# Performance work log

Hardware: AMD Instinct MI355X
Metric: run time of the kernel (lower is better)

Reference implementation:

```python
import jax, jax.numpy as jnp
import numpy as np

B, D, V = 2048, 512, 50304


def setup_inputs() -> dict:
    key = jax.random.key(0)
    ks = jax.random.split(key, 7)
    scale = 1.0 / np.sqrt(D)
    return {
        "student_h": jax.random.normal(ks[0], (B, D), dtype=jnp.float32) * scale,
        "student_c": jax.random.normal(ks[1], (V, D), dtype=jnp.float32) * scale,
        "teacher_h": jax.random.normal(ks[2], (B, D), dtype=jnp.float32) * scale,
        "teacher_c": jax.random.normal(ks[3], (V, D), dtype=jnp.float32) * scale,
        "ce_coeff": jax.random.uniform(ks[4], (B,), dtype=jnp.float32),
        "kl_coeff": jax.random.uniform(ks[5], (B,), dtype=jnp.float32),
        "targets": jax.random.randint(ks[6], (B,), 0, V, dtype=jnp.int64),
    }


def reference(student_h, student_c, teacher_h, teacher_c, ce_coeff, kl_coeff, targets):
    # Fused linear head: student/teacher logits over the full vocab  [B, V]
    s_logits = jnp.einsum("bd,vd->bv", student_h, student_c)
    t_logits = jnp.einsum("bd,vd->bv", teacher_h, teacher_c)

    s_lse = jax.nn.logsumexp(s_logits, axis=1)  # [B]
    t_lse = jax.nn.logsumexp(t_logits, axis=1)  # [B]

    # Cross-entropy per row: lse - logit[target]
    tgt_logit = jnp.take_along_axis(s_logits, targets[:, None], axis=1)[:, 0]
    ce = s_lse - tgt_logit  # [B]

    # KL(teacher || student) per row
    log_ps = s_logits - s_lse[:, None]
    log_pt = t_logits - t_lse[:, None]
    pt = jnp.exp(log_pt)
    kl = jnp.sum(pt * (log_pt - log_ps), axis=1)  # [B]

    # Per-row coefficients absorb any reduction weighting (as in the kernel)
    loss = jnp.sum(ce_coeff * ce + kl_coeff * kl)
    return loss
```

## Files before the change

kernel.cpp:

```cpp
#include <hip/hip_runtime.h>
#include <hip/hip_fp8.h>

#define B_ 2048
#define D_ 512
#define V_ 50304
#define NROWB 16
#define NCOLB 393
#define NWG (NROWB * NCOLB)
#define NCOPY 32
#define LOG2E 1.44269504088896340736f
#define LN2 0.69314718055994530942f

typedef __attribute__((ext_vector_type(16))) float f32x16;
typedef __attribute__((ext_vector_type(8))) int v8i;
typedef unsigned char u8;

__device__ inline unsigned f2bf(float f) {
  unsigned u = __float_as_uint(f);
  u += 0x7fffu + ((u >> 16) & 1u);
  return u >> 16;
}

__global__ void cast8t_kernel(const float* __restrict__ src, uint4* __restrict__ dst,
                              float scale, int nchunk) {
  int i = blockIdx.x * blockDim.x + threadIdx.x;
  if (i >= nchunk) return;
  int c = i & 127;
  int h = (i >> 7) & 1;
  int kc = (i >> 8) & 7;
  int p = i >> 11;
  const float4* s = (const float4*)(src + (size_t)(p * 128 + c) * 512 + kc * 64 + h * 32);
  union { u8 b[32]; uint4 u[2]; } o;
#pragma unroll
  for (int q = 0; q < 8; ++q) {
    float4 f = s[q];
    o.b[q * 4 + 0] = __hip_fp8_e4m3(f.x * scale).__x;
    o.b[q * 4 + 1] = __hip_fp8_e4m3(f.y * scale).__x;
    o.b[q * 4 + 2] = __hip_fp8_e4m3(f.z * scale).__x;
    o.b[q * 4 + 3] = __hip_fp8_e4m3(f.w * scale).__x;
  }
  dst[2 * i] = o.u[0];
  dst[2 * i + 1] = o.u[1];
}

__global__ void cast8_kernel(const float* __restrict__ src, uint2* __restrict__ dst,
                             float scale, int n8) {
  int i = blockIdx.x * blockDim.x + threadIdx.x;
  int stride = gridDim.x * blockDim.x;
  const float4* s4 = (const float4*)src;
  for (; i < n8; i += stride) {
    float4 a = s4[2 * i], b = s4[2 * i + 1];
    union { u8 c[8]; uint2 u; } p;
    p.c[0] = __hip_fp8_e4m3(a.x * scale).__x;
    p.c[1] = __hip_fp8_e4m3(a.y * scale).__x;
    p.c[2] = __hip_fp8_e4m3(a.z * scale).__x;
    p.c[3] = __hip_fp8_e4m3(a.w * scale).__x;
    p.c[4] = __hip_fp8_e4m3(b.x * scale).__x;
    p.c[5] = __hip_fp8_e4m3(b.y * scale).__x;
    p.c[6] = __hip_fp8_e4m3(b.z * scale).__x;
    p.c[7] = __hip_fp8_e4m3(b.w * scale).__x;
    dst[i] = p.u;
  }
}

__global__ void tgt_kernel(const float* __restrict__ sh, const float* __restrict__ sc,
                           const int* __restrict__ targets, float* __restrict__ tgt_out) {
  int gid = blockIdx.x * blockDim.x + threadIdx.x;
  int w = gid >> 6, lane = gid & 63;
  if (w >= B_) return;
  int tgt = targets[w];
  const float4* a = (const float4*)(sh + (size_t)w * D_);
  const float4* b = (const float4*)(sc + (size_t)tgt * D_);
  float acc = 0.f;
#pragma unroll
  for (int i = 0; i < 2; ++i) {
    float4 x = a[lane + i * 64], y = b[lane + i * 64];
    acc += x.x * y.x + x.y * y.y + x.z * y.z + x.w * y.w;
  }
#pragma unroll
  for (int off = 1; off < 64; off <<= 1) acc += __shfl_xor(acc, off);
  if (lane == 0) tgt_out[w] = acc;
}

__global__ __launch_bounds__(512, 4) void lce_main(
    const u8* __restrict__ SH8, const u8* __restrict__ TH8,
    const u8* __restrict__ SC8t, const u8* __restrict__ TC8t,
    float* __restrict__ stats32) {
  __shared__ __align__(16) uint exch[8192];
  __shared__ float pss[2][2][64];
  __shared__ float pst[2][2][64];
  __shared__ float pat[2][2][64];

  const int tid = threadIdx.x;
  const int lane = tid & 63, w = tid >> 6;
  const int wq = w & 3;
  const int mat = w >> 2;
  const int wr = wq >> 1;
  const int wc = wq & 1;
  const int l5 = lane & 31;
  const int hi = lane >> 5;

  const int hw = blockIdx.x;
  const int lid = (hw & 7) * 786 + (hw >> 3);
  const int row0 = (lid & 15) * 128;
  const int p = lid >> 4;
  const int jcopy = (hw & 7) * 4 + (p & 3);
  float* stats = stats32 + (size_t)jcopy * B_ * 3;

  const u8* gA = (mat ? TH8 : SH8) + (size_t)(row0 + wr * 64 + l5) * D_ + hi * 32;
  const u8* gB = (mat ? TC8t : SC8t) + (size_t)p * 65536 + hi * 4096 + (wc * 64 + l5) * 32;

  f32x16 acc[2][2];
#pragma unroll
  for (int mi = 0; mi < 2; ++mi)
#pragma unroll
    for (int ni = 0; ni < 2; ++ni)
#pragma unroll
      for (int e = 0; e < 16; ++e) acc[mi][ni][e] = 0.f;

#pragma unroll
  for (int kc = 0; kc < 8; ++kc) {
    v8i av[2], bv[2];
#pragma unroll
    for (int mi = 0; mi < 2; ++mi)
      av[mi] = *(const v8i*)(gA + (size_t)(mi * 32) * D_ + kc * 64);
#pragma unroll
    for (int ni = 0; ni < 2; ++ni)
      bv[ni] = *(const v8i*)(gB + kc * 8192 + ni * 1024);

    __builtin_amdgcn_s_setprio(1);
#pragma unroll
    for (int mi = 0; mi < 2; ++mi)
#pragma unroll
      for (int ni = 0; ni < 2; ++ni)
        acc[mi][ni] = __builtin_amdgcn_mfma_scale_f32_32x32x64_f8f6f4(
            av[mi], bv[ni], acc[mi][ni], 0, 0, 0, 127, 0, 127);
    __builtin_amdgcn_s_setprio(0);
  }

  const float inv = 1.0f / 256.0f;

  if (mat == 0) {
#pragma unroll
    for (int mi = 0; mi < 2; ++mi)
#pragma unroll
      for (int ni = 0; ni < 2; ++ni)
#pragma unroll
        for (int rp = 0; rp < 8; ++rp) {
          uint u = f2bf(acc[mi][ni][2 * rp] * inv) |
                   (f2bf(acc[mi][ni][2 * rp + 1] * inv) << 16);
          exch[(((wq * 2 + mi) * 2 + ni) * 8 + rp) * 64 + lane] = u;
        }
  }
  __syncthreads();

  if (mat == 0) {
#pragma unroll
    for (int mi = 0; mi < 2; ++mi)
#pragma unroll
      for (int rp = 0; rp < 8; ++rp) {
        float v0 = __builtin_amdgcn_exp2f(acc[mi][0][2 * rp] * inv) +
                   __builtin_amdgcn_exp2f(acc[mi][1][2 * rp] * inv);
        float v1 = __builtin_amdgcn_exp2f(acc[mi][0][2 * rp + 1] * inv) +
                   __builtin_amdgcn_exp2f(acc[mi][1][2 * rp + 1] * inv);
#pragma unroll
        for (int off = 1; off < 32; off <<= 1) {
          v0 += __shfl_xor(v0, off);
          v1 += __shfl_xor(v1, off);
        }
        if (l5 == 0) {
          int r0 = ((2 * rp) & 3) + 8 * (rp >> 1) + 4 * hi + mi * 32;
          pss[wr][wc][r0] = v0;
          pss[wr][wc][r0 + 1] = v1;
        }
      }
  } else {
#pragma unroll
    for (int mi = 0; mi < 2; ++mi)
#pragma unroll
      for (int rp = 0; rp < 8; ++rp) {
        float st0 = 0.f, st1 = 0.f, at0 = 0.f, at1 = 0.f;
#pragma unroll
        for (int ni = 0; ni < 2; ++ni) {
          uint u = exch[(((wq * 2 + mi) * 2 + ni) * 8 + rp) * 64 + lane];
          float sv0 = __uint_as_float(u << 16);
          float sv1 = __uint_as_float(u & 0xffff0000u);
          float t0 = acc[mi][ni][2 * rp] * inv;
          float t1 = acc[mi][ni][2 * rp + 1] * inv;
          float e0 = __builtin_amdgcn_exp2f(t0);
          float e1 = __builtin_amdgcn_exp2f(t1);
          st0 += e0; st1 += e1;
          at0 += e0 * (t0 - sv0);
          at1 += e1 * (t1 - sv1);
        }
#pragma unroll
        for (int off = 1; off < 32; off <<= 1) {
          st0 += __shfl_xor(st0, off);
          st1 += __shfl_xor(st1, off);
          at0 += __shfl_xor(at0, off);
          at1 += __shfl_xor(at1, off);
        }
        if (l5 == 0) {
          int r0 = ((2 * rp) & 3) + 8 * (rp >> 1) + 4 * hi + mi * 32;
          pst[wr][wc][r0] = st0;
          pst[wr][wc][r0 + 1] = st1;
          pat[wr][wc][r0] = at0;
          pat[wr][wc][r0 + 1] = at1;
        }
      }
  }
  __syncthreads();

  if (wc == 0) {
    int row = row0 + wr * 64 + lane;
    if (mat == 0) {
      float ss = pss[wr][0][lane] + pss[wr][1][lane];
      atomicAdd(&stats[(size_t)row * 3 + 0], ss);
    } else {
      float st = pst[wr][0][lane] + pst[wr][1][lane];
      float at = pat[wr][0][lane] + pat[wr][1][lane];
      atomicAdd(&stats[(size_t)row * 3 + 1], st);
      atomicAdd(&stats[(size_t)row * 3 + 2], at);
    }
  }
}

__global__ void finalize(const float* __restrict__ stats32, const float* __restrict__ tgt,
                         const float* __restrict__ cec, const float* __restrict__ klc,
                         float* __restrict__ out) {
  __shared__ float red[16];
  int tid = threadIdx.x;
  float acc = 0.f;
  for (int r = tid; r < B_; r += 1024) {
    float ss = 0.f, st = 0.f, at = 0.f;
#pragma unroll
    for (int j = 0; j < NCOPY; ++j) {
      const float* s = stats32 + ((size_t)j * B_ + r) * 3;
      ss += s[0]; st += s[1]; at += s[2];
    }
    float s_lse = LN2 * __builtin_amdgcn_logf(ss);
    float t_lse = LN2 * __builtin_amdgcn_logf(st);
    float kl = s_lse - t_lse + LN2 * at / st;
    float ce = s_lse - tgt[r];
    acc += cec[r] * ce + klc[r] * kl;
  }
#pragma unroll
  for (int off = 1; off < 64; off <<= 1) acc += __shfl_xor(acc, off);
  if ((tid & 63) == 0) red[tid >> 6] = acc;
  __syncthreads();
  if (tid == 0) {
    float s = 0.f;
#pragma unroll
    for (int i = 0; i < 16; ++i) s += red[i];
    out[0] = s;
  }
}

extern "C" void kernel_launch(void* const* d_in, const int* in_sizes, int n_in,
                              void* d_out, int out_size, void* d_ws, size_t ws_size,
                              hipStream_t stream) {
  const float* sh = (const float*)d_in[0];
  const float* sc = (const float*)d_in[1];
  const float* th = (const float*)d_in[2];
  const float* tc = (const float*)d_in[3];
  const float* cec = (const float*)d_in[4];
  const float* klc = (const float*)d_in[5];
  const int* targets = (const int*)d_in[6];
  float* out = (float*)d_out;

  char* ws = (char*)d_ws;
  u8* SC8t = (u8*)ws;
  u8* TC8t = SC8t + (size_t)V_ * D_;
  u8* SH8 = TC8t + (size_t)V_ * D_;
  u8* TH8 = SH8 + (size_t)B_ * D_;
  float* stats32 = (float*)(TH8 + (size_t)B_ * D_);
  float* tgt = stats32 + (size_t)NCOPY * B_ * 3;

  hipMemsetAsync(stats32, 0, (size_t)NCOPY * B_ * 3 * sizeof(float), stream);
  const float hscale = 16.0f * LOG2E;
  const float cscale = 16.0f;
  const int nchunk = V_ * D_ / 32;
  cast8t_kernel<<<3144, 256, 0, stream>>>(sc, (uint4*)SC8t, cscale, nchunk);
  cast8t_kernel<<<3144, 256, 0, stream>>>(tc, (uint4*)TC8t, cscale, nchunk);
  cast8_kernel<<<256, 256, 0, stream>>>(sh, (uint2*)SH8, hscale, B_ * D_ / 8);
  cast8_kernel<<<256, 256, 0, stream>>>(th, (uint2*)TH8, hscale, B_ * D_ / 8);
  tgt_kernel<<<512, 256, 0, stream>>>(sh, sc, targets, tgt);

  lce_main<<<NWG, 512, 0, stream>>>(SH8, TH8, SC8t, TC8t, stats32);
  finalize<<<1, 1024, 0, stream>>>(stats32, tgt, cec, klc, out);
}
```

Before: 318.6 us.

## Fuse student/teacher GEMMs per wave with LDS double-buffered vocab tiles

The main kernel moves from 512-thread blocks, where separate waves computed the student and teacher tiles and swapped bf16 logits through LDS, to 256-thread blocks in which each wave computes both the student and teacher accumulators for the same tile. The epilogue then needs no cross-wave exchange. Each block now covers three vocab panels in sequence. Vocab tiles are staged into double-buffered LDS with global_load_lds, using manual vmcnt waits and barriers, and the hidden-state matrices use the same transposed fp8 layout so the cast kernel can be reused. This removes the bf16 rounding of student logits and the LDS exchange, and amortises block launch. In exchange it roughly doubles accumulator register pressure, issues more atomics per wave, and depends on hand-written waitcnt counts being correct.

Measured after the change: 1.103 ms. 3.46x slower.

```diff
diff --git a/kernel.cpp b/kernel.cpp
--- a/kernel.cpp
+++ b/kernel.cpp
@@ -4,9 +4,8 @@
 #define B_ 2048
 #define D_ 512
 #define V_ 50304
-#define NROWB 16
-#define NCOLB 393
-#define NWG (NROWB * NCOLB)
+#define NPG 131
+#define NWG (16 * NPG)
 #define NCOPY 32
 #define LOG2E 1.44269504088896340736f
 #define LN2 0.69314718055994530942f
@@ -15,10 +14,9 @@
 typedef __attribute__((ext_vector_type(8))) int v8i;
 typedef unsigned char u8;
 
-__device__ inline unsigned f2bf(float f) {
-  unsigned u = __float_as_uint(f);
-  u += 0x7fffu + ((u >> 16) & 1u);
-  return u >> 16;
+__device__ inline void gload16(const void* g, void* l) {
+  __builtin_amdgcn_global_load_lds((const __attribute__((address_space(1))) void*)g,
+                                   (__attribute__((address_space(3))) void*)l, 16, 0, 0);
 }
 
 __global__ void cast8t_kernel(const float* __restrict__ src, uint4* __restrict__ dst,
@@ -43,26 +41,6 @@
   dst[2 * i + 1] = o.u[1];
 }
 
-__global__ void cast8_kernel(const float* __restrict__ src, uint2* __restrict__ dst,
-                             float scale, int n8) {
-  int i = blockIdx.x * blockDim.x + threadIdx.x;
-  int stride = gridDim.x * blockDim.x;
-  const float4* s4 = (const float4*)src;
-  for (; i < n8; i += stride) {
-    float4 a = s4[2 * i], b = s4[2 * i + 1];
-    union { u8 c[8]; uint2 u; } p;
-    p.c[0] = __hip_fp8_e4m3(a.x * scale).__x;
-    p.c[1] = __hip_fp8_e4m3(a.y * scale).__x;
-    p.c[2] = __hip_fp8_e4m3(a.z * scale).__x;
-    p.c[3] = __hip_fp8_e4m3(a.w * scale).__x;
-    p.c[4] = __hip_fp8_e4m3(b.x * scale).__x;
-    p.c[5] = __hip_fp8_e4m3(b.y * scale).__x;
-    p.c[6] = __hip_fp8_e4m3(b.z * scale).__x;
-    p.c[7] = __hip_fp8_e4m3(b.w * scale).__x;
-    dst[i] = p.u;
-  }
-}
-
 __global__ void tgt_kernel(const float* __restrict__ sh, const float* __restrict__ sc,
                            const int* __restrict__ targets, float* __restrict__ tgt_out) {
   int gid = blockIdx.x * blockDim.x + threadIdx.x;
@@ -82,145 +60,123 @@
   if (lane == 0) tgt_out[w] = acc;
 }
 
-__global__ __launch_bounds__(512, 4) void lce_main(
-    const u8* __restrict__ SH8, const u8* __restrict__ TH8,
+__global__ __launch_bounds__(256, 2) void lce_main(
+    const u8* __restrict__ SH8t, const u8* __restrict__ TH8t,
     const u8* __restrict__ SC8t, const u8* __restrict__ TC8t,
     float* __restrict__ stats32) {
-  __shared__ __align__(16) uint exch[8192];
-  __shared__ float pss[2][2][64];
-  __shared__ float pst[2][2][64];
-  __shared__ float pat[2][2][64];
+  __shared__ __align__(16) u8 smem[2][2][8192];
 
   const int tid = threadIdx.x;
   const int lane = tid & 63, w = tid >> 6;
-  const int wq = w & 3;
-  const int mat = w >> 2;
-  const int wr = wq >> 1;
-  const int wc = wq & 1;
-  const int l5 = lane & 31;
-  const int hi = lane >> 5;
+  const int wr = w >> 1, wc = w & 1;
+  const int l5 = lane & 31, hi = lane >> 5;
 
   const int hw = blockIdx.x;
-  const int lid = (hw & 7) * 786 + (hw >> 3);
+  const int lid = (hw & 7) * (NWG / 8) + (hw >> 3);
   const int row0 = (lid & 15) * 128;
-  const int p = lid >> 4;
-  const int jcopy = (hw & 7) * 4 + (p & 3);
+  const int pg = lid >> 4;
+  const int jcopy = (hw & 7) * 4 + (pg & 3);
   float* stats = stats32 + (size_t)jcopy * B_ * 3;
 
-  const u8* gA = (mat ? TH8 : SH8) + (size_t)(row0 + wr * 64 + l5) * D_ + hi * 32;
-  const u8* gB = (mat ? TC8t : SC8t) + (size_t)p * 65536 + hi * 4096 + (wc * 64 + l5) * 32;
-
-  f32x16 acc[2][2];
-#pragma unroll
-  for (int mi = 0; mi < 2; ++mi)
-#pragma unroll
-    for (int ni = 0; ni < 2; ++ni)
-#pragma unroll
-      for (int e = 0; e < 16; ++e) acc[mi][ni][e] = 0.f;
-
-#pragma unroll
-  for (int kc = 0; kc < 8; ++kc) {
-    v8i av[2], bv[2];
+  const int pA = lid & 15;
+  const u8* gAs = SH8t + (size_t)pA * 65536 + hi * 4096 + wr * 2048 + l5 * 32;
+  const u8* gAt = TH8t + (size_t)pA * 65536 + hi * 4096 + wr * 2048 + l5 * 32;
+  const u8* gBs = SC8t + tid * 16;
+  const u8* gBt = TC8t + tid * 16;
+  const int bbase = hi * 4096 + wc * 2048 + l5 * 32;
+
+  f32x16 accS[2][2], accT[2][2];
+  v8i aS[2], aT[2];
+
+#define STAGE(buf, poff)                                                      \
+  {                                                                           \
+    gload16(gBs + (poff), &smem[buf][0][tid * 16]);                           \
+    gload16(gBs + (poff) + 4096, &smem[buf][0][4096 + tid * 16]);             \
+    gload16(gBt + (poff), &smem[buf][1][tid * 16]);                           \
+    gload16(gBt + (poff) + 4096, &smem[buf][1][4096 + tid * 16]);             \
+  }
+
+#define LOADA(pq, kc)                                                         \
+  {                                                                           \
+    aS[0] = *(const v8i*)(gAs + (kc) * 8192);                                 \
+    aS[1] = *(const v8i*)(gAs + (kc) * 8192 + 1024);                          \
+    aT[0] = *(const v8i*)(gAt + (kc) * 8192);                                 \
+    aT[1] = *(const v8i*)(gAt + (kc) * 8192 + 1024);                          \
+  }
+
+  const float inv = 1.0f / 256.0f;
+
+  STAGE(0, (size_t)(pg * 3) * 65536);
+
+  for (int pp = 0; pp < 3; ++pp) {
+    const size_t pbase = (size_t)(pg * 3 + pp) * 65536;
 #pragma unroll
     for (int mi = 0; mi < 2; ++mi)
-      av[mi] = *(const v8i*)(gA + (size_t)(mi * 32) * D_ + kc * 64);
-#pragma unroll
-    for (int ni = 0; ni < 2; ++ni)
-      bv[ni] = *(const v8i*)(gB + kc * 8192 + ni * 1024);
-
-    __builtin_amdgcn_s_setprio(1);
-#pragma unroll
-    for (int mi = 0; mi < 2; ++mi)
 #pragma unroll
       for (int ni = 0; ni < 2; ++ni)
-        acc[mi][ni] = __builtin_amdgcn_mfma_scale_f32_32x32x64_f8f6f4(
-            av[mi], bv[ni], acc[mi][ni], 0, 0, 0, 127, 0, 127);
-    __builtin_amdgcn_s_setprio(0);
-  }
-
-  const float inv = 1.0f / 256.0f;
-
-  if (mat == 0) {
-#pragma unroll
-    for (int mi = 0; mi < 2; ++mi)
-#pragma unroll
-      for (int ni = 0; ni < 2; ++ni)
-#pragma unroll
-        for (int rp = 0; rp < 8; ++rp) {
-          uint u = f2bf(acc[mi][ni][2 * rp] * inv) |
-                   (f2bf(acc[mi][ni][2 * rp + 1] * inv) << 16);
-          exch[(((wq * 2 + mi) * 2 + ni) * 8 + rp) * 64 + lane] = u;
-        }
-  }
-  __syncthreads();
-
-  if (mat == 0) {
-#pragma unroll
-    for (int mi = 0; mi < 2; ++mi)
-#pragma unroll
-      for (int rp = 0; rp < 8; ++rp) {
-        float v0 = __builtin_amdgcn_exp2f(acc[mi][0][2 * rp] * inv) +
-                   __builtin_amdgcn_exp2f(acc[mi][1][2 * rp] * inv);
-        float v1 = __builtin_amdgcn_exp2f(acc[mi][0][2 * rp + 1] * inv) +
-                   __builtin_amdgcn_exp2f(acc[mi][1][2 * rp + 1] * inv);
+#pragma unroll
+        for (int e = 0; e < 16; ++e) { accS[mi][ni][e] = 0.f; accT[mi][ni][e] = 0.f; }
+
+#pragma unroll
+    for (int kc = 0; kc < 8; ++kc) {
+      const int buf = kc & 1;
+      LOADA(pp, kc);
+      if (kc < 7) {
+        STAGE(buf ^ 1, pbase + (kc + 1) * 8192);
+        asm volatile("s_waitcnt vmcnt(12)\n\ts_barrier" ::: "memory");
+      } else if (pp < 2) {
+        STAGE(0, pbase + 65536);
+        asm volatile("s_waitcnt vmcnt(12)\n\ts_barrier" ::: "memory");
+      } else {
+        asm volatile("s_waitcnt vmcnt(8)\n\ts_barrier" ::: "memory");
+      }
+
+      v8i bS[2], bT[2];
+#pragma unroll
+      for (int ni = 0; ni < 2; ++ni) {
+        bS[ni] = *(const v8i*)&smem[buf][0][bbase + ni * 1024];
+        bT[ni] = *(const v8i*)&smem[buf][1][bbase + ni * 1024];
+      }
+#pragma unroll
+      for (int mi = 0; mi < 2; ++mi)
+#pragma unroll
+        for (int ni = 0; ni < 2; ++ni) {
+          accS[mi][ni] = __builtin_amdgcn_mfma_scale_f32_32x32x64_f8f6f4(
+              aS[mi], bS[ni], accS[mi][ni], 0, 0, 0, 127, 0, 127);
+          accT[mi][ni] = __builtin_amdgcn_mfma_scale_f32_32x32x64_f8f6f4(
+              aT[mi], bT[ni], accT[mi][ni], 0, 0, 0, 127, 0, 127);
+        }
+      asm volatile("s_barrier" ::: "memory");
+    }
+
+#pragma unroll
+    for (int mi = 0; mi < 2; ++mi) {
+#pragma unroll
+      for (int reg = 0; reg < 16; ++reg) {
+        float ss = 0.f, st = 0.f, at = 0.f;
+#pragma unroll
+        for (int ni = 0; ni < 2; ++ni) {
+          float sv = accS[mi][ni][reg] * inv;
+          float tv = accT[mi][ni][reg] * inv;
+          float es = __builtin_amdgcn_exp2f(sv);
+          float et = __builtin_amdgcn_exp2f(tv);
+          ss += es;
+          st += et;
+          at += et * (tv - sv);
+        }
 #pragma unroll
         for (int off = 1; off < 32; off <<= 1) {
-          v0 += __shfl_xor(v0, off);
-          v1 += __shfl_xor(v1, off);
+          ss += __shfl_xor(ss, off);
+          st += __shfl_xor(st, off);
+          at += __shfl_xor(at, off);
         }
         if (l5 == 0) {
-          int r0 = ((2 * rp) & 3) + 8 * (rp >> 1) + 4 * hi + mi * 32;
-          pss[wr][wc][r0] = v0;
-          pss[wr][wc][r0 + 1] = v1;
+          int row = row0 + wr * 64 + mi * 32 + (reg & 3) + 8 * (reg >> 2) + 4 * hi;
+          atomicAdd(&stats[(size_t)row * 3 + 0], ss);
+          atomicAdd(&stats[(size_t)row * 3 + 1], st);
+          atomicAdd(&stats[(size_t)row * 3 + 2], at);
         }
       }
-  } else {
-#pragma unroll
-    for (int mi = 0; mi < 2; ++mi)
-#pragma unroll
-      for (int rp = 0; rp < 8; ++rp) {
-        float st0 = 0.f, st1 = 0.f, at0 = 0.f, at1 = 0.f;
-#pragma unroll
-        for (int ni = 0; ni < 2; ++ni) {
-          uint u = exch[(((wq * 2 + mi) * 2 + ni) * 8 + rp) * 64 + lane];
-          float sv0 = __uint_as_float(u << 16);
-          float sv1 = __uint_as_float(u & 0xffff0000u);
-          float t0 = acc[mi][ni][2 * rp] * inv;
-          float t1 = acc[mi][ni][2 * rp + 1] * inv;
-          float e0 = __builtin_amdgcn_exp2f(t0);
-          float e1 = __builtin_amdgcn_exp2f(t1);
-          st0 += e0; st1 += e1;
-          at0 += e0 * (t0 - sv0);
-          at1 += e1 * (t1 - sv1);
-        }
-#pragma unroll
-        for (int off = 1; off < 32; off <<= 1) {
-          st0 += __shfl_xor(st0, off);
-          st1 += __shfl_xor(st1, off);
-          at0 += __shfl_xor(at0, off);
-          at1 += __shfl_xor(at1, off);
-        }
-        if (l5 == 0) {
-          int r0 = ((2 * rp) & 3) + 8 * (rp >> 1) + 4 * hi + mi * 32;
-          pst[wr][wc][r0] = st0;
-          pst[wr][wc][r0 + 1] = st1;
-          pat[wr][wc][r0] = at0;
-          pat[wr][wc][r0 + 1] = at1;
-        }
-      }
-  }
-  __syncthreads();
-
-  if (wc == 0) {
-    int row = row0 + wr * 64 + lane;
-    if (mat == 0) {
-      float ss = pss[wr][0][lane] + pss[wr][1][lane];
-      atomicAdd(&stats[(size_t)row * 3 + 0], ss);
-    } else {
-      float st = pst[wr][0][lane] + pst[wr][1][lane];
-      float at = pat[wr][0][lane] + pat[wr][1][lane];
-      atomicAdd(&stats[(size_t)row * 3 + 1], st);
-      atomicAdd(&stats[(size_t)row * 3 + 2], at);
     }
   }
 }
@@ -271,21 +227,22 @@
   char* ws = (char*)d_ws;
   u8* SC8t = (u8*)ws;
   u8* TC8t = SC8t + (size_t)V_ * D_;
-  u8* SH8 = TC8t + (size_t)V_ * D_;
-  u8* TH8 = SH8 + (size_t)B_ * D_;
-  float* stats32 = (float*)(TH8 + (size_t)B_ * D_);
+  u8* SH8t = TC8t + (size_t)V_ * D_;
+  u8* TH8t = SH8t + (size_t)B_ * D_;
+  float* stats32 = (float*)(TH8t + (size_t)B_ * D_);
   float* tgt = stats32 + (size_t)NCOPY * B_ * 3;
 
   hipMemsetAsync(stats32, 0, (size_t)NCOPY * B_ * 3 * sizeof(float), stream);
   const float hscale = 16.0f * LOG2E;
   const float cscale = 16.0f;
-  const int nchunk = V_ * D_ / 32;
-  cast8t_kernel<<<3144, 256, 0, stream>>>(sc, (uint4*)SC8t, cscale, nchunk);
-  cast8t_kernel<<<3144, 256, 0, stream>>>(tc, (uint4*)TC8t, cscale, nchunk);
-  cast8_kernel<<<256, 256, 0, stream>>>(sh, (uint2*)SH8, hscale, B_ * D_ / 8);
-  cast8_kernel<<<256, 256, 0, stream>>>(th, (uint2*)TH8, hscale, B_ * D_ / 8);
+  const int ncC = V_ * D_ / 32;
+  const int ncH = B_ * D_ / 32;
+  cast8t_kernel<<<(ncC + 255) / 256, 256, 0, stream>>>(sc, (uint4*)SC8t, cscale, ncC);
+  cast8t_kernel<<<(ncC + 255) / 256, 256, 0, stream>>>(tc, (uint4*)TC8t, cscale, ncC);
+  cast8t_kernel<<<(ncH + 255) / 256, 256, 0, stream>>>(sh, (uint4*)SH8t, hscale, ncH);
+  cast8t_kernel<<<(ncH + 255) / 256, 256, 0, stream>>>(th, (uint4*)TH8t, hscale, ncH);
   tgt_kernel<<<512, 256, 0, stream>>>(sh, sc, targets, tgt);
 
-  lce_main<<<NWG, 512, 0, stream>>>(SH8, TH8, SC8t, TC8t, stats32);
+  lce_main<<<NWG, 256, 0, stream>>>(SH8t, TH8t, SC8t, TC8t, stats32);
   finalize<<<1, 1024, 0, stream>>>(stats32, tgt, cec, klc, out);
 }
```
